# Kernel tuning notes

Measured on AMD Instinct MI355X. Metric: run time of the kernel, lower is better.

## Reference

```python
import jax, jax.numpy as jnp
import numpy as np

B, L, ENC, DEC, ATT = 64, 1024, 1024, 1024, 1024


def setup_inputs() -> dict:
    key = jax.random.key(0)
    ks = jax.random.split(key, 8)
    s1 = 1.0 / np.sqrt(ENC)
    s2 = 1.0 / np.sqrt(DEC)
    s3 = 1.0 / np.sqrt(ATT)
    return {
        "features": jax.random.normal(ks[0], (B, L, ENC), jnp.float32),
        "hidden_state": jax.random.normal(ks[1], (B, DEC), jnp.float32),
        "W1_w": jax.random.uniform(ks[2], (ENC, ATT), jnp.float32, -s1, s1),
        "W1_b": jax.random.uniform(ks[3], (ATT,), jnp.float32, -s1, s1),
        "W2_w": jax.random.uniform(ks[4], (DEC, ATT), jnp.float32, -s2, s2),
        "W2_b": jax.random.uniform(ks[5], (ATT,), jnp.float32, -s2, s2),
        "V_w": jax.random.uniform(ks[6], (ATT,), jnp.float32, -s3, s3),
        "V_b": jax.random.uniform(ks[7], (), jnp.float32, -s3, s3),
    }


def reference(features, hidden_state, W1_w, W1_b, W2_w, W2_b, V_w, V_b):
    # proj_f: [B, L, ATT]; proj_h: [B, 1, ATT]
    proj_f = jnp.einsum('ble,ea->bla', features, W1_w) + W1_b
    proj_h = (hidden_state @ W2_w + W2_b)[:, None, :]
    scores = jnp.tanh(proj_f + proj_h) @ V_w + V_b  # [B, L]
    alpha = jax.nn.softmax(scores, axis=1)
    context = jnp.einsum('bl,ble->be', alpha, features)
    return alpha, context
```

## Files before the change

kernel.cpp:

```cpp
#include <hip/hip_runtime.h>
#include <hip/hip_bf16.h>


typedef __bf16 bf16x8 __attribute__((ext_vector_type(8)));
typedef float floatx4 __attribute__((ext_vector_type(4)));
typedef unsigned short ushort_t;
typedef unsigned long long u64;

__device__ __forceinline__ ushort_t f2b(float x) {
    union { float f; unsigned u; } v; v.f = x;
    unsigned r = (v.u + 0x7fffu + ((v.u >> 16) & 1u)) >> 16;
    return (ushort_t)r;
}

__device__ __forceinline__ float b2f(ushort_t u) {
    union { unsigned u; float f; } v; v.u = (unsigned)u << 16; return v.f;
}

__device__ __forceinline__ u64 pack4(float4 f) {
    return (u64)f2b(f.x) | ((u64)f2b(f.y) << 16) |
           ((u64)f2b(f.z) << 32) | ((u64)f2b(f.w) << 48);
}

__device__ __forceinline__ void gload_lds16(const void* g, void* l) {
    __builtin_amdgcn_global_load_lds(
        (const __attribute__((address_space(1))) void*)g,
        (__attribute__((address_space(3))) void*)l, 16, 0, 0);
}

__device__ __forceinline__ float fast_tanh(float x) {
    const float ax = fabsf(x);
    const float t  = __expf(-2.0f * ax);
    const float r  = (1.0f - t) * __builtin_amdgcn_rcpf(1.0f + t);
    return copysignf(r, x);
}

#define LOG2E2 2.885390082f

__global__ __launch_bounds__(256) void convert_feat_kernel(
    const float* __restrict__ feat, ushort_t* __restrict__ featb) {
    const size_t idx = ((size_t)blockIdx.x * 256 + threadIdx.x) * 8;
    const float4 f0 = *(const float4*)(feat + idx);
    const float4 f1 = *(const float4*)(feat + idx + 4);
    *(u64*)(featb + idx)     = pack4(f0);
    *(u64*)(featb + idx + 4) = pack4(f1);
}

__global__ __launch_bounds__(256) void transpose_w1_kernel(
    const float* __restrict__ w1, ushort_t* __restrict__ w1t) {
    __shared__ ushort_t tile[64][65];
    const int k0 = blockIdx.x * 64, n0 = blockIdx.y * 64;
    const int tr = threadIdx.x >> 6;
    const int tc = threadIdx.x & 63;
#pragma unroll
    for (int i = 0; i < 16; i++) {
        int r = i * 4 + tr;
        tile[tc][r] = f2b(w1[(size_t)(k0 + r) * 1024 + n0 + tc]);
    }
    __syncthreads();
#pragma unroll
    for (int i = 0; i < 16; i++) {
        int r = i * 4 + tr;
        w1t[(size_t)(n0 + r) * 1024 + k0 + tc] = tile[r][tc];
    }
}

__global__ __launch_bounds__(256) void projh_kernel(
    const float* __restrict__ hidden, const float* __restrict__ w2,
    const float* __restrict__ w2b, const float* __restrict__ w1b,
    float* __restrict__ ph) {
    const int b  = blockIdx.y;
    const int al = threadIdx.x & 63;
    const int eg = threadIdx.x >> 6;
    const int a  = blockIdx.x * 64 + al;
    const float* h = hidden + b * 1024;
    float sum = 0.f;
    const int e0 = eg * 256;
#pragma unroll 8
    for (int e = e0; e < e0 + 256; e++)
        sum += h[e] * w2[(size_t)e * 1024 + a];
    __shared__ float red[256];
    red[threadIdx.x] = sum;
    __syncthreads();
    if (threadIdx.x < 64)
        ph[b * 1024 + a] = w2b[a] + w1b[a] + red[al] + red[al + 64] +
                           red[al + 128] + red[al + 192];
}


#define WAITV(n) asm volatile("s_waitcnt vmcnt(" #n ")" ::: "memory")
#define BAR() __builtin_amdgcn_s_barrier()

#define STG_A(d, h, kc) do { \
    gload_lds16(aSrc + (kc) + (h) * 32,          aDst + (d) * 16384 + (h) * 8192); \
    gload_lds16(aSrc + 131072 + (kc) + (h) * 32, aDst + (d) * 16384 + (h) * 8192 + 4096); \
  } while (0)
#define STG_B(d, h, kc) do { \
    gload_lds16(bSrc + (kc) + (h) * 32,          bDst + (d) * 16384 + (h) * 8192); \
    gload_lds16(bSrc + 131072 + (kc) + (h) * 32, bDst + (d) * 16384 + (h) * 8192 + 4096); \
  } while (0)

#define PHASE(d, h, mq, LOADB) do { \
    bf16x8 af[4]; \
    _Pragma("unroll") \
    for (int i_ = 0; i_ < 4; i_++) \
      af[i_] = *(const bf16x8*)(As + (d) * 16384 + (h) * 8192 + \
                                (ga + (mq) * 4 + i_) * 512 + rdo); \
    if (LOADB) { \
      _Pragma("unroll") \
      for (int j_ = 0; j_ < 4; j_++) \
        bf[j_] = *(const bf16x8*)(Bs + (d) * 16384 + (h) * 8192 + \
                                  (gb + j_) * 512 + rdo); \
    } \
    __builtin_amdgcn_s_setprio(1); \
    _Pragma("unroll") \
    for (int i_ = 0; i_ < 4; i_++) \
      _Pragma("unroll") \
      for (int j_ = 0; j_ < 4; j_++) \
        acc[(mq) * 4 + i_][j_] = __builtin_amdgcn_mfma_f32_16x16x32_bf16( \
            af[i_], bf[j_], acc[(mq) * 4 + i_][j_], 0, 0, 0); \
    __builtin_amdgcn_s_setprio(0); \
  } while (0)

#define TILE(t, d) do { \
    const int k1_ = (((t) + 1) & 15) * 64; \
    const int k2_ = (((t) + 2) & 15) * 64; \
    STG_A(d ^ 1, 1, k1_); \
    PHASE(d, 0, 0, 1); \
    STG_B(d ^ 1, 1, k1_); \
    PHASE(d, 0, 1, 0); \
    WAITV(8); BAR(); \
    STG_A(d, 0, k2_); \
    PHASE(d, 1, 0, 1); \
    STG_B(d, 0, k2_); \
    PHASE(d, 1, 1, 0); \
    WAITV(8); BAR(); \
  } while (0)

__global__ __launch_bounds__(512, 2) void gemm_scores_256_kernel(
    const ushort_t* __restrict__ featb,
    const ushort_t* __restrict__ w1t,
    const float* __restrict__ ph,
    const float* __restrict__ vw,
    float* __restrict__ part) {
    __shared__ ushort_t As[2 * 16384];
    __shared__ ushort_t Bs[2 * 16384];
    __shared__ float cbias[256];
    __shared__ float vvw[256];

    const int tid = threadIdx.x;
    const int orig = blockIdx.x;
    const int wgid = (orig & 7) * 128 + (orig >> 3);
    const int nt = wgid & 3;
    const int mt = wgid >> 2;
    const int n0 = nt * 256;
    const int m0 = mt * 256;
    const int b  = m0 >> 10;

    if (tid < 256) {
        cbias[tid] = ph[(b << 10) + n0 + tid];
        vvw[tid]   = vw[n0 + tid];
    }

    const int w    = tid >> 6;
    const int lane = tid & 63;
    const int q    = lane >> 4;
    const int l15  = lane & 15;
    const int rdo  = l15 * 32 + ((q ^ ((l15 >> 1) & 3)) << 3);
    const int ga   = (w >> 2) * 8;
    const int gb   = (w & 3) * 4;
    const int sb   = ((lane & 3) ^ ((lane >> 3) & 3)) << 3;

    const ushort_t* aSrc = featb + (size_t)(m0 + w * 16 + (lane >> 2)) * 1024 + sb;
    const ushort_t* bSrc = w1t  + (size_t)(n0 + w * 16 + (lane >> 2)) * 1024 + sb;
    ushort_t* aDst = As + w * 512;
    ushort_t* bDst = Bs + w * 512;

    floatx4 acc[8][4] = {};
    bf16x8 bf[4];

    STG_A(0, 0, 0);  STG_B(0, 0, 0);
    STG_A(0, 1, 0);  STG_B(0, 1, 0);
    STG_A(1, 0, 64); STG_B(1, 0, 64);
    WAITV(8); BAR();

    for (int it = 0; it < 8; it++) {
        TILE(2 * it,     0);
        TILE(2 * it + 1, 1);
    }
    WAITV(0);

    float vv[4], cbk[4];
    float sum_vvw = 0.f;
#pragma unroll
    for (int j = 0; j < 4; j++) {
        const int col = (w & 3) * 64 + j * 16 + l15;
        vv[j]  = vvw[col];
        cbk[j] = LOG2E2 * cbias[col];
        sum_vvw += vv[j];
    }
    const int slot  = nt * 4 + (w & 3);
    const int rbase = m0 + (w >> 2) * 128;
#pragma unroll
    for (int mf = 0; mf < 8; mf++) {
#pragma unroll
        for (int r = 0; r < 4; r++) {
            const int row = rbase + mf * 16 + q * 4 + r;
            float s2 = 0.f;
#pragma unroll
            for (int j = 0; j < 4; j++) {
                const float arg = fmaf(LOG2E2, acc[mf][j][r], cbk[j]);
                const float e   = __builtin_amdgcn_exp2f(arg);
                s2 = fmaf(__builtin_amdgcn_rcpf(1.0f + e), vv[j], s2);
            }
            float s = fmaf(-2.0f, s2, sum_vvw);
            s += __shfl_xor(s, 1);
            s += __shfl_xor(s, 2);
            s += __shfl_xor(s, 4);
            s += __shfl_xor(s, 8);
            if (l15 == 0) part[slot * 65536 + row] = s;
        }
    }
}

__global__ __launch_bounds__(1024) void softmax_context_kernel(
    const float* __restrict__ part, const ushort_t* __restrict__ featb,
    float* __restrict__ alpha, float* __restrict__ ctx) {
    const int b   = blockIdx.y;
    const int tid = threadIdx.x;
    __shared__ float red1[1024];
    __shared__ float al_lds[1024];
    __shared__ floatx4 red4[16 * 64];

    float s = 0.f;
    const int m = b * 1024 + tid;
#pragma unroll
    for (int nb = 0; nb < 16; nb++) s += part[nb * 65536 + m];

    red1[tid] = s;
    __syncthreads();
    for (int st = 512; st > 0; st >>= 1) {
        if (tid < st) red1[tid] = fmaxf(red1[tid], red1[tid + st]);
        __syncthreads();
    }
    const float mx = red1[0];
    __syncthreads();

    const float v = __expf(s - mx);
    red1[tid] = v;
    __syncthreads();
    for (int st = 512; st > 0; st >>= 1) {
        if (tid < st) red1[tid] += red1[tid + st];
        __syncthreads();
    }
    const float av = v * (1.0f / red1[0]);
    al_lds[tid] = av;
    if (blockIdx.x == 0) alpha[m] = av;
    __syncthreads();

    const int el = tid & 63, lg = tid >> 6;
    const int e  = blockIdx.x * 256 + el * 4;
    const ushort_t* fb = featb + ((size_t)b << 20) + e;
    floatx4 acc = {};
    const int l0 = lg * 64;
#pragma unroll 4
    for (int l = l0; l < l0 + 64; l++) {
        const float a = al_lds[l];
        const ushort4 u = *(const ushort4*)(fb + (size_t)l * 1024);
        acc[0] = fmaf(a, b2f(u.x), acc[0]);
        acc[1] = fmaf(a, b2f(u.y), acc[1]);
        acc[2] = fmaf(a, b2f(u.z), acc[2]);
        acc[3] = fmaf(a, b2f(u.w), acc[3]);
    }
    red4[lg * 64 + el] = acc;
    __syncthreads();
#pragma unroll
    for (int st = 8; st > 0; st >>= 1) {
        if (lg < st) red4[lg * 64 + el] += red4[(lg + st) * 64 + el];
        __syncthreads();
    }
    if (lg == 0)
        *(floatx4*)(ctx + b * 1024 + e) = red4[el];
}

__global__ __launch_bounds__(256) void softmax_kernel(
    const float* __restrict__ part, float* __restrict__ alpha) {
    const int b = blockIdx.x;
    const int tid = threadIdx.x;
    __shared__ float red[256];
    float v[4];
    float mx = -1e30f;
#pragma unroll
    for (int i = 0; i < 4; i++) {
        const int m = b * 1024 + tid + i * 256;
        float s = 0.f;
#pragma unroll
        for (int nb = 0; nb < 16; nb++) s += part[nb * 65536 + m];
        v[i] = s;
        mx = fmaxf(mx, s);
    }
    red[tid] = mx; __syncthreads();
    for (int s = 128; s > 0; s >>= 1) {
        if (tid < s) red[tid] = fmaxf(red[tid], red[tid + s]);
        __syncthreads();
    }
    mx = red[0]; __syncthreads();
    float sum = 0.f;
#pragma unroll
    for (int i = 0; i < 4; i++) { v[i] = __expf(v[i] - mx); sum += v[i]; }
    red[tid] = sum; __syncthreads();
    for (int s = 128; s > 0; s >>= 1) {
        if (tid < s) red[tid] += red[tid + s];
        __syncthreads();
    }
    const float inv = 1.0f / red[0];
#pragma unroll
    for (int i = 0; i < 4; i++)
        alpha[b * 1024 + tid + i * 256] = v[i] * inv;
}

__global__ __launch_bounds__(1024) void context_kernel(
    const float* __restrict__ alpha, const float* __restrict__ feat,
    float* __restrict__ ctx) {
    const int b  = blockIdx.y;
    const int el = threadIdx.x & 63;
    const int lg = threadIdx.x >> 6;
    const int e  = blockIdx.x * 256 + el * 4;
    const float* fb = feat + (size_t)b * 1024 * 1024;
    const float* ab = alpha + b * 1024;
    floatx4 acc = {};
    const int l0 = lg * 64;
#pragma unroll 4
    for (int l = l0; l < l0 + 64; l++) {
        const float a = ab[l];
        const floatx4 f = *(const floatx4*)(fb + (size_t)l * 1024 + e);
        acc += a * f;
    }
    __shared__ floatx4 red[16 * 64];
    red[lg * 64 + el] = acc;
    __syncthreads();
#pragma unroll
    for (int s = 8; s > 0; s >>= 1) {
        if (lg < s) red[lg * 64 + el] += red[(lg + s) * 64 + el];
        __syncthreads();
    }
    if (lg == 0)
        *(floatx4*)(ctx + b * 1024 + e) = red[el];
}

#define KP 72
__global__ __launch_bounds__(256) void gemm_scores_f32_kernel(
    const float* __restrict__ feat, const ushort_t* __restrict__ w1t,
    const float* __restrict__ ph, const float* __restrict__ vw,
    float* __restrict__ part) {
    __shared__ ushort_t Asf[128 * KP];
    __shared__ ushort_t Bsf[128 * KP];
    __shared__ float cbias[128];
    __shared__ float vvw[128];
    const int tid = threadIdx.x;
    const int nt = blockIdx.x, n0 = nt * 128, m0 = blockIdx.y * 128;
    const int b = m0 >> 10;
    if (tid < 128) { cbias[tid] = ph[(b << 10) + n0 + tid]; vvw[tid] = vw[n0 + tid]; }
    const int wave = tid >> 6, lane = tid & 63;
    const int wr = (wave >> 1) * 64, wc = (wave & 1) * 64;
    const int q = lane >> 4, l15 = lane & 15;
    floatx4 acc[4][4] = {};
    const int arow = tid >> 4, acol = (tid & 15) * 4;
    const int brow = tid >> 3, bcol = (tid & 7) * 8;
    const float* aptr = feat + (size_t)m0 * 1024;
    const ushort_t* bptr = w1t + (size_t)n0 * 1024;
    for (int kt = 0; kt < 1024; kt += 64) {
#pragma unroll
        for (int p = 0; p < 8; p++) {
            int r = p * 16 + arow;
            const float4 f = *(const float4*)(aptr + (size_t)r * 1024 + kt + acol);
            *(u64*)&Asf[r * KP + acol] = pack4(f);
        }
#pragma unroll
        for (int p = 0; p < 4; p++) {
            int r = p * 32 + brow;
            *(uint4*)&Bsf[r * KP + bcol] =
                *(const uint4*)(bptr + (size_t)r * 1024 + kt + bcol);
        }
        __syncthreads();
#pragma unroll
        for (int ks = 0; ks < 64; ks += 32) {
            bf16x8 af[4], bfr[4];
#pragma unroll
            for (int t = 0; t < 4; t++)
                af[t] = *(const bf16x8*)&Asf[(wr + t * 16 + l15) * KP + ks + q * 8];
#pragma unroll
            for (int t = 0; t < 4; t++)
                bfr[t] = *(const bf16x8*)&Bsf[(wc + t * 16 + l15) * KP + ks + q * 8];
#pragma unroll
            for (int tm = 0; tm < 4; tm++)
#pragma unroll
                for (int tn = 0; tn < 4; tn++)
                    acc[tm][tn] = __builtin_amdgcn_mfma_f32_16x16x32_bf16(
                        af[tm], bfr[tn], acc[tm][tn], 0, 0, 0);
        }
        __syncthreads();
    }
    const int slot = nt * 2 + (wave & 1);
#pragma unroll
    for (int tm = 0; tm < 4; tm++) {
#pragma unroll
        for (int r = 0; r < 4; r++) {
            const int row = wr + tm * 16 + q * 4 + r;
            float s = 0.f;
#pragma unroll
            for (int tn = 0; tn < 4; tn++) {
                const int col = wc + tn * 16 + l15;
                s += fast_tanh(acc[tm][tn][r] + cbias[col]) * vvw[col];
            }
            s += __shfl_xor(s, 1);
            s += __shfl_xor(s, 2);
            s += __shfl_xor(s, 4);
            s += __shfl_xor(s, 8);
            if (l15 == 0) part[slot * 65536 + m0 + row] = s;
        }
    }
}

extern "C" void kernel_launch(void* const* d_in, const int* in_sizes, int n_in,
                              void* d_out, int out_size, void* d_ws, size_t ws_size,
                              hipStream_t stream) {
    const float* feat = (const float*)d_in[0];
    const float* hid  = (const float*)d_in[1];
    const float* w1w  = (const float*)d_in[2];
    const float* w1b  = (const float*)d_in[3];
    const float* w2w  = (const float*)d_in[4];
    const float* w2b  = (const float*)d_in[5];
    const float* vw   = (const float*)d_in[6];

    const size_t FEATB_BYTES = (size_t)64 * 1024 * 1024 * 2;
    const size_t W1T_BYTES   = (size_t)1024 * 1024 * 2;
    const size_t PH_BYTES    = (size_t)64 * 1024 * 4;
    const size_t PART_BYTES  = (size_t)16 * 65536 * 4;
    const bool   big_ws = ws_size >= FEATB_BYTES + W1T_BYTES + PH_BYTES + PART_BYTES;
    if (!big_ws && ws_size < W1T_BYTES + PH_BYTES + PART_BYTES) return;

    char* ws = (char*)d_ws;
    ushort_t* featb = (ushort_t*)ws;
    size_t off = big_ws ? FEATB_BYTES : 0;
    ushort_t* w1t  = (ushort_t*)(ws + off);
    float* ph      = (float*)(ws + off + W1T_BYTES);
    float* part    = (float*)(ws + off + W1T_BYTES + PH_BYTES);

    float* alpha = (float*)d_out;
    float* ctx   = alpha + 64 * 1024;

    transpose_w1_kernel<<<dim3(16, 16), 256, 0, stream>>>(w1w, w1t);
    projh_kernel<<<dim3(16, 64), 256, 0, stream>>>(hid, w2w, w2b, w1b, ph);
    if (big_ws) {
        convert_feat_kernel<<<32768, 256, 0, stream>>>(feat, featb);
        gemm_scores_256_kernel<<<dim3(1024), 512, 0, stream>>>(
            featb, w1t, ph, vw, part);
        softmax_context_kernel<<<dim3(4, 64), 1024, 0, stream>>>(
            part, featb, alpha, ctx);
    } else {
        gemm_scores_f32_kernel<<<dim3(8, 512), 256, 0, stream>>>(
            feat, w1t, ph, vw, part);
        softmax_kernel<<<64, 256, 0, stream>>>(part, alpha);
        context_kernel<<<dim3(4, 64), 1024, 0, stream>>>(alpha, feat, ctx);
    }
}
```

Measured before the change: 578.6 us.

## Split GEMM tile across 16 waves with 1024 threads per block

The 256x256 score GEMM tile is now computed by 16 waves of 1024 threads instead of 8 waves of 512. Each wave handles a 64x64 sub-tile with a 4x4 accumulator array, and each thread issues a single LDS staging load per half-tile. This halves per-thread accumulator registers and raises wave count per block. The cost is that B fragments are reloaded every phase, barriers sync more waves, and only one block fits per CU.

```diff
diff --git a/kernel.cpp b/kernel.cpp
--- a/kernel.cpp
+++ b/kernel.cpp
@@ -91,34 +91,28 @@
 #define WAITV(n) asm volatile("s_waitcnt vmcnt(" #n ")" ::: "memory")
 #define BAR() __builtin_amdgcn_s_barrier()
 
-#define STG_A(d, h, kc) do { \
-    gload_lds16(aSrc + (kc) + (h) * 32,          aDst + (d) * 16384 + (h) * 8192); \
-    gload_lds16(aSrc + 131072 + (kc) + (h) * 32, aDst + (d) * 16384 + (h) * 8192 + 4096); \
-  } while (0)
-#define STG_B(d, h, kc) do { \
-    gload_lds16(bSrc + (kc) + (h) * 32,          bDst + (d) * 16384 + (h) * 8192); \
-    gload_lds16(bSrc + 131072 + (kc) + (h) * 32, bDst + (d) * 16384 + (h) * 8192 + 4096); \
-  } while (0)
-
-#define PHASE(d, h, mq, LOADB) do { \
-    bf16x8 af[4]; \
+#define STG_A(d, h, kc) \
+    gload_lds16(aSrc + (kc) + (h) * 32, aDst + (d) * 16384 + (h) * 8192)
+#define STG_B(d, h, kc) \
+    gload_lds16(bSrc + (kc) + (h) * 32, bDst + (d) * 16384 + (h) * 8192)
+
+#define PHASE(d, h) do { \
+    bf16x8 af[4], bfr[4]; \
     _Pragma("unroll") \
     for (int i_ = 0; i_ < 4; i_++) \
       af[i_] = *(const bf16x8*)(As + (d) * 16384 + (h) * 8192 + \
-                                (ga + (mq) * 4 + i_) * 512 + rdo); \
-    if (LOADB) { \
-      _Pragma("unroll") \
-      for (int j_ = 0; j_ < 4; j_++) \
-        bf[j_] = *(const bf16x8*)(Bs + (d) * 16384 + (h) * 8192 + \
-                                  (gb + j_) * 512 + rdo); \
-    } \
+                                (ga + i_) * 512 + rdo); \
+    _Pragma("unroll") \
+    for (int j_ = 0; j_ < 4; j_++) \
+      bfr[j_] = *(const bf16x8*)(Bs + (d) * 16384 + (h) * 8192 + \
+                                 (gb + j_) * 512 + rdo); \
     __builtin_amdgcn_s_setprio(1); \
     _Pragma("unroll") \
     for (int i_ = 0; i_ < 4; i_++) \
       _Pragma("unroll") \
       for (int j_ = 0; j_ < 4; j_++) \
-        acc[(mq) * 4 + i_][j_] = __builtin_amdgcn_mfma_f32_16x16x32_bf16( \
-            af[i_], bf[j_], acc[(mq) * 4 + i_][j_], 0, 0, 0); \
+        acc[i_][j_] = __builtin_amdgcn_mfma_f32_16x16x32_bf16( \
+            af[i_], bfr[j_], acc[i_][j_], 0, 0, 0); \
     __builtin_amdgcn_s_setprio(0); \
   } while (0)
 
@@ -126,18 +120,16 @@
     const int k1_ = (((t) + 1) & 15) * 64; \
     const int k2_ = (((t) + 2) & 15) * 64; \
     STG_A(d ^ 1, 1, k1_); \
-    PHASE(d, 0, 0, 1); \
+    PHASE(d, 0); \
     STG_B(d ^ 1, 1, k1_); \
-    PHASE(d, 0, 1, 0); \
-    WAITV(8); BAR(); \
+    WAITV(4); BAR(); \
     STG_A(d, 0, k2_); \
-    PHASE(d, 1, 0, 1); \
+    PHASE(d, 1); \
     STG_B(d, 0, k2_); \
-    PHASE(d, 1, 1, 0); \
-    WAITV(8); BAR(); \
+    WAITV(4); BAR(); \
   } while (0)
 
-__global__ __launch_bounds__(512, 2) void gemm_scores_256_kernel(
+__global__ __launch_bounds__(1024) void gemm_scores_256_kernel(
     const ushort_t* __restrict__ featb,
     const ushort_t* __restrict__ w1t,
     const float* __restrict__ ph,
@@ -167,7 +159,7 @@
     const int q    = lane >> 4;
     const int l15  = lane & 15;
     const int rdo  = l15 * 32 + ((q ^ ((l15 >> 1) & 3)) << 3);
-    const int ga   = (w >> 2) * 8;
+    const int ga   = (w >> 2) * 4;
     const int gb   = (w & 3) * 4;
     const int sb   = ((lane & 3) ^ ((lane >> 3) & 3)) << 3;
 
@@ -176,13 +168,12 @@
     ushort_t* aDst = As + w * 512;
     ushort_t* bDst = Bs + w * 512;
 
-    floatx4 acc[8][4] = {};
-    bf16x8 bf[4];
+    floatx4 acc[4][4] = {};
 
     STG_A(0, 0, 0);  STG_B(0, 0, 0);
     STG_A(0, 1, 0);  STG_B(0, 1, 0);
     STG_A(1, 0, 64); STG_B(1, 0, 64);
-    WAITV(8); BAR();
+    WAITV(4); BAR();
 
     for (int it = 0; it < 8; it++) {
         TILE(2 * it,     0);
@@ -200,9 +191,9 @@
         sum_vvw += vv[j];
     }
     const int slot  = nt * 4 + (w & 3);
-    const int rbase = m0 + (w >> 2) * 128;
-#pragma unroll
-    for (int mf = 0; mf < 8; mf++) {
+    const int rbase = m0 + (w >> 2) * 64;
+#pragma unroll
+    for (int mf = 0; mf < 4; mf++) {
 #pragma unroll
         for (int r = 0; r < 4; r++) {
             const int row = rbase + mf * 16 + q * 4 + r;
@@ -454,7 +445,7 @@
     projh_kernel<<<dim3(16, 64), 256, 0, stream>>>(hid, w2w, w2b, w1b, ph);
     if (big_ws) {
         convert_feat_kernel<<<32768, 256, 0, stream>>>(feat, featb);
-        gemm_scores_256_kernel<<<dim3(1024), 512, 0, stream>>>(
+        gemm_scores_256_kernel<<<dim3(1024), 1024, 0, stream>>>(
             featb, w1t, ph, vw, part);
         softmax_context_kernel<<<dim3(4, 64), 1024, 0, stream>>>(
             part, featb, alpha, ctx);
```

After: 573.7 us. About the same (-0.8%).
